# Performance work log

Measured on AMD Instinct MI355X. Metric: run time of the kernel, lower is better.

## Reference

```python
import jax, jax.numpy as jnp
import numpy as np

B, P, ENC = 64, 196, 512
E, H, A, V, L = 1024, 1024, 512, 20000, 25


def setup_inputs() -> dict:
    key = jax.random.key(0)
    ks = jax.random.split(key, 20)
    s = 0.02
    return {
        "encoder_out": jax.random.normal(ks[0], (B, P, ENC), jnp.float32),
        "captions": jax.random.randint(ks[1], (B, L), 0, V),
        "lengths": L,
        # attention MLP
        "W_enc_att": jax.random.normal(ks[2], (ENC, A), jnp.float32) * s,
        "b_enc_att": jnp.zeros((A,), jnp.float32),
        "W_dec_att": jax.random.normal(ks[3], (H, A), jnp.float32) * s,
        "b_dec_att": jnp.zeros((A,), jnp.float32),
        "W_full_att": jax.random.normal(ks[4], (A, 1), jnp.float32) * s,
        "b_full_att": jnp.zeros((1,), jnp.float32),
        # embedding
        "emb_table": jax.random.normal(ks[5], (V, E), jnp.float32) * s,
        # LSTMCell: input = embedding + context -> (E+ENC, 4H)
        "W_ih": jax.random.normal(ks[6], (E + ENC, 4 * H), jnp.float32) * s,
        "b_ih": jnp.zeros((4 * H,), jnp.float32),
        "W_hh": jax.random.normal(ks[7], (H, 4 * H), jnp.float32) * s,
        "b_hh": jnp.zeros((4 * H,), jnp.float32),
        # init states
        "W_init_h": jax.random.normal(ks[8], (ENC, H), jnp.float32) * s,
        "b_init_h": jnp.zeros((H,), jnp.float32),
        "W_init_c": jax.random.normal(ks[9], (ENC, H), jnp.float32) * s,
        "b_init_c": jnp.zeros((H,), jnp.float32),
        # gate + output proj
        "W_fbeta": jax.random.normal(ks[10], (H, ENC), jnp.float32) * s,
        "b_fbeta": jnp.zeros((ENC,), jnp.float32),
        "W_fc": jax.random.normal(ks[11], (H, V), jnp.float32) * s,
        "b_fc": jnp.zeros((V,), jnp.float32),
    }


def _decode(encoder_out, W_enc_att, b_enc_att, W_dec_att, b_dec_att,
            W_full_att, b_full_att, emb_table, W_ih, b_ih, W_hh, b_hh,
            W_init_h, b_init_h, W_init_c, b_init_c, W_fbeta, b_fbeta,
            W_fc, b_fc, captions, T):
    # precompute encoder-side attention projection (constant across timesteps)
    att_enc = encoder_out @ W_enc_att + b_enc_att          # (B, P, A)
    mean_feat = encoder_out.mean(axis=1)                   # (B, ENC)
    h0 = mean_feat @ W_init_h + b_init_h
    c0 = mean_feat @ W_init_c + b_init_c
    embeddings = emb_table[captions[:, :T]]                # (B, T, E)
    xs = jnp.swapaxes(embeddings, 0, 1)                    # (T, B, E)

    def step(carry, emb_t):
        h, c = carry
        att_dec = h @ W_dec_att + b_dec_att                # (B, A)
        energy = (jax.nn.relu(att_enc + att_dec[:, None, :]) @ W_full_att
                  + b_full_att)[..., 0]                    # (B, P)
        alpha = jax.nn.softmax(energy, axis=1)
        context = jnp.einsum('bp,bpe->be', alpha, encoder_out)
        gate = jax.nn.sigmoid(h @ W_fbeta + b_fbeta)       # (B, ENC)
        x = jnp.concatenate([emb_t, gate * context], axis=1)
        gates = x @ W_ih + b_ih + h @ W_hh + b_hh          # (B, 4H)
        i, f, g, o = jnp.split(gates, 4, axis=1)           # torch order i,f,g,o
        c = jax.nn.sigmoid(f) * c + jax.nn.sigmoid(i) * jnp.tanh(g)
        h = jax.nn.sigmoid(o) * jnp.tanh(c)
        preds = h @ W_fc + b_fc                            # dropout = identity (eval)
        return (h, c), (preds, alpha)

    _, (preds, alphas) = jax.lax.scan(step, (h0, c0), xs)
    predictions = jnp.swapaxes(preds, 0, 1)                # (B, T, V)
    alphas = jnp.swapaxes(alphas, 0, 1)                    # (B, T, P)
    return predictions, alphas


def reference(encoder_out, captions, lengths, W_enc_att, b_enc_att, W_dec_att,
              b_dec_att, W_full_att, b_full_att, emb_table, W_ih, b_ih, W_hh,
              b_hh, W_init_h, b_init_h, W_init_c, b_init_c, W_fbeta, b_fbeta,
              W_fc, b_fc):
    T = int(lengths) - 1
    return _decode(encoder_out, W_enc_att, b_enc_att, W_dec_att, b_dec_att,
                   W_full_att, b_full_att, emb_table, W_ih, b_ih, W_hh, b_hh,
                   W_init_h, b_init_h, W_init_c, b_init_c, W_fbeta, b_fbeta,
                   W_fc, b_fc, captions, T)
```

## Files before the change

### kernel.cpp

```cpp
#include <hip/hip_runtime.h>
#include <hip/hip_bf16.h>

#define BB 64
#define PP 196
#define ENCD 512
#define ED 1024
#define HD 1024
#define AD 512
#define VD 20000
#define TT 24
#define VPAD 20096
#define NS 8

typedef __attribute__((ext_vector_type(8))) short short8;
typedef __attribute__((ext_vector_type(4))) short short4v;
typedef __attribute__((ext_vector_type(4))) float f32x4;

__device__ __forceinline__ unsigned short f2bf(float f) {
    unsigned u = __builtin_bit_cast(unsigned, f);
    u = (u + 0x7FFFu + ((u >> 16) & 1u)) >> 16;
    return (unsigned short)u;
}
__device__ __forceinline__ void split2(float v, unsigned short& h, unsigned short& l) {
    h = f2bf(v);
    float hf = __builtin_bit_cast(float, ((unsigned)h) << 16);
    l = f2bf(v - hf);
}

__global__ __launch_bounds__(256) void split_w_kernel(
    const float* __restrict__ W, unsigned short* __restrict__ oh,
    unsigned short* __restrict__ ol, int N, int Npad, int coff, int Nlaunch) {
    int n = blockIdx.x * 256 + threadIdx.x;
    if (n >= Nlaunch) return;
    int kc = blockIdx.y;
    short8 vh, vl;
    #pragma unroll
    for (int j = 0; j < 8; ++j) {
        float v = (n < N) ? W[(size_t)(kc * 8 + j) * N + n] : 0.f;
        unsigned short h, l; split2(v, h, l);
        vh[j] = (short)h; vl[j] = (short)l;
    }
    size_t o = ((size_t)kc * Npad + coff + n) * 8;
    *(short8*)(oh + o) = vh; *(short8*)(ol + o) = vl;
}

__global__ __launch_bounds__(128) void embed_split_kernel(
    const int* __restrict__ captions, const float* __restrict__ table,
    unsigned short* __restrict__ eh, unsigned short* __restrict__ el) {
    int t = blockIdx.x, b = blockIdx.y;
    int kc = threadIdx.x;
    int tok = captions[b * 25 + t];
    const float* row = table + (size_t)tok * ED;
    short8 vh, vl;
    #pragma unroll
    for (int j = 0; j < 8; ++j) {
        unsigned short h, l; split2(row[kc * 8 + j], h, l);
        vh[j] = (short)h; vl[j] = (short)l;
    }
    size_t o = ((size_t)t * 128 * 64 + (size_t)kc * 64 + b) * 8;
    *(short8*)(eh + o) = vh; *(short8*)(el + o) = vl;
}

__global__ __launch_bounds__(512) void mean_kernel(const float* __restrict__ enc,
                                                   float* __restrict__ mf) {
    int b = blockIdx.x; int e = threadIdx.x;
    const float* base = enc + (size_t)b * PP * ENCD + e;
    float s = 0.f;
    #pragma unroll 4
    for (int p = 0; p < PP; ++p) s += base[(size_t)p * ENCD];
    mf[b * ENCD + e] = s * (1.f / PP);
}

__global__ __launch_bounds__(256) void init_hc_kernel(
    const float* __restrict__ mf,
    const float* __restrict__ Wh, const float* __restrict__ bh,
    const float* __restrict__ Wc, const float* __restrict__ bc,
    unsigned short* __restrict__ hc_h, unsigned short* __restrict__ hc_l,
    float* __restrict__ c0) {
    int b = blockIdx.x;
    int isC = blockIdx.y;
    const float* W    = isC ? Wc : Wh;
    const float* bias = isC ? bc : bh;
    __shared__ float smf[ENCD];
    for (int i = threadIdx.x; i < ENCD; i += 256) smf[i] = mf[b * ENCD + i];
    __syncthreads();
    #pragma unroll
    for (int jj = 0; jj < 4; ++jj) {
        int j = threadIdx.x + jj * 256;
        float acc = bias[j];
        for (int k = 0; k < ENCD; ++k) acc += smf[k] * W[(size_t)k * HD + j];
        if (isC) c0[b * HD + j] = acc;
        else {
            unsigned short h, l; split2(acc, h, l);
            size_t o = ((size_t)(j >> 3) * 64 + b) * 8 + (j & 7);
            hc_h[o] = h; hc_l[o] = l;
        }
    }
}

__global__ __launch_bounds__(256) void mfma_gemm_bigf(
    const float* __restrict__ Ap,
    const unsigned short* __restrict__ Bh, const unsigned short* __restrict__ Bl,
    const float* __restrict__ bias, float* __restrict__ C,
    int N, int Npad, int K, int Mtiles, int Ntiles, int inner_m) {
    __shared__ __align__(16) short lds[32768];
    short* Ahs = lds;
    short* Als = lds + 8192;
    short* Bhs = lds + 16384;
    short* Bls = lds + 24576;
    int tid = threadIdx.x, lane = tid & 63, w = tid >> 6;
    int nwg = Mtiles * Ntiles;
    int orig = blockIdx.x;
    int q = nwg >> 3, r = nwg & 7;
    int xcd = orig & 7;
    int basew = (xcd < r) ? xcd * (q + 1) : r * (q + 1) + (xcd - r) * q;
    int wg = basew + (orig >> 3);
    int mt, nt;
    if (inner_m) { mt = wg % Mtiles; nt = wg / Mtiles; }
    else         { nt = wg % Ntiles; mt = wg / Ntiles; }
    int m0 = mt * 128, n0 = nt * 128;
    int wr = w >> 1, wc = w & 1;
    f32x4 acc[4][4];
    #pragma unroll
    for (int i = 0; i < 4; ++i)
        #pragma unroll
        for (int j = 0; j < 4; ++j) acc[i][j] = (f32x4){0.f, 0.f, 0.f, 0.f};
    int nsteps = K >> 6;
    float4 va[8];
    short8 rb[2][4];
    auto load_step = [&](int s) {
        int k0 = s * 64, kc0 = s * 8;
        #pragma unroll
        for (int it = 0; it < 8; ++it) {
            int idx = it * 256 + tid; int m = idx >> 4, k4 = idx & 15;
            va[it] = *(const float4*)(Ap + (size_t)(m0 + m) * K + k0 + k4 * 4);
        }
        #pragma unroll
        for (int it = 0; it < 4; ++it) {
            int g = w * 4 + it; int kcl = g >> 1; int rb0 = (g & 1) * 64;
            size_t gb = ((size_t)(kc0 + kcl) * Npad + n0 + rb0 + lane) * 8;
            rb[0][it] = *(const short8*)(Bh + gb);
            rb[1][it] = *(const short8*)(Bl + gb);
        }
    };
    load_step(0);
    for (int s = 0; s < nsteps; ++s) {
        __syncthreads();
        #pragma unroll
        for (int it = 0; it < 8; ++it) {
            int idx = it * 256 + tid; int m = idx >> 4, k4 = idx & 15;
            int kc = k4 >> 1, jh = (k4 & 1) * 4;
            float vv[4] = {va[it].x, va[it].y, va[it].z, va[it].w};
            short4v hv, lv;
            #pragma unroll
            for (int qq = 0; qq < 4; ++qq) {
                unsigned short h, l; split2(vv[qq], h, l);
                hv[qq] = (short)h; lv[qq] = (short)l;
            }
            int o = kc * 1024 + ((m ^ kc) << 3) + jh;
            *(short4v*)(Ahs + o) = hv;
            *(short4v*)(Als + o) = lv;
        }
        #pragma unroll
        for (int it = 0; it < 4; ++it) {
            int g = w * 4 + it; int kcl = g >> 1; int rb0 = (g & 1) * 64;
            int o = (kcl * 128 + rb0 + lane) * 8;
            *(short8*)(Bhs + o) = rb[0][it];
            *(short8*)(Bls + o) = rb[1][it];
        }
        __syncthreads();
        if (s + 1 < nsteps) load_step(s + 1);
        #pragma unroll
        for (int ks = 0; ks < 2; ++ks) {
            int kq = ks * 4 + (lane >> 4);
            short8 afh[4], afl[4], bfh[4], bfl[4];
            #pragma unroll
            for (int mi = 0; mi < 4; ++mi) {
                int row = wr * 64 + mi * 16 + (lane & 15);
                int o = kq * 1024 + ((row ^ kq) << 3);
                afh[mi] = *(const short8*)(Ahs + o);
                afl[mi] = *(const short8*)(Als + o);
            }
            #pragma unroll
            for (int ni = 0; ni < 4; ++ni) {
                int o = (kq * 128 + wc * 64 + ni * 16 + (lane & 15)) * 8;
                bfh[ni] = *(const short8*)(Bhs + o);
                bfl[ni] = *(const short8*)(Bls + o);
            }
            #pragma unroll
            for (int mi = 0; mi < 4; ++mi)
                #pragma unroll
                for (int ni = 0; ni < 4; ++ni) {
                    acc[mi][ni] = __builtin_amdgcn_mfma_f32_16x16x32_bf16(afh[mi], bfh[ni], acc[mi][ni], 0, 0, 0);
                    acc[mi][ni] = __builtin_amdgcn_mfma_f32_16x16x32_bf16(afh[mi], bfl[ni], acc[mi][ni], 0, 0, 0);
                    acc[mi][ni] = __builtin_amdgcn_mfma_f32_16x16x32_bf16(afl[mi], bfh[ni], acc[mi][ni], 0, 0, 0);
                }
        }
    }
    #pragma unroll
    for (int mi = 0; mi < 4; ++mi) {
        int rrow = m0 + wr * 64 + mi * 16 + ((lane >> 4) << 2);
        #pragma unroll
        for (int ni = 0; ni < 4; ++ni) {
            int c = n0 + wc * 64 + ni * 16 + (lane & 15);
            if (c < N) {
                float bv = bias ? bias[c] : 0.f;
                #pragma unroll
                for (int qq = 0; qq < 4; ++qq)
                    C[(size_t)(rrow + qq) * N + c] = acc[mi][ni][qq] + bv;
            }
        }
    }
}

__global__ __launch_bounds__(256) void mfma_gemm_small(
    const unsigned short* __restrict__ A0h, const unsigned short* __restrict__ A0l,
    const unsigned short* __restrict__ A1h, const unsigned short* __restrict__ A1l,
    const unsigned short* __restrict__ A2h, const unsigned short* __restrict__ A2l,
    int c0, int c1,
    const unsigned short* __restrict__ B0h, const unsigned short* __restrict__ B0l,
    const unsigned short* __restrict__ B1h, const unsigned short* __restrict__ B1l,
    int bc0, float* __restrict__ out, int Npad, int steps) {
    __shared__ __align__(16) short lds[24576];
    short* Ahs = lds;
    short* Als = lds + 4096;
    short* Bhs = lds + 8192;
    short* Bls = lds + 16384;
    int tid = threadIdx.x, lane = tid & 63, w = tid >> 6;
    int n0 = blockIdx.x * 128;
    int kc_base = blockIdx.y * steps * 8;
    out += (size_t)blockIdx.y * 64 * Npad;
    f32x4 acc[4][2];
    #pragma unroll
    for (int i = 0; i < 4; ++i)
        #pragma unroll
        for (int j = 0; j < 2; ++j) acc[i][j] = (f32x4){0.f, 0.f, 0.f, 0.f};
    short8 raa[2][2], rbb[2][4];
    auto load_step = [&](int s) {
        int kc0 = kc_base + s * 8;
        #pragma unroll
        for (int it = 0; it < 2; ++it) {
            int kcl = w * 2 + it; int kcg = kc0 + kcl;
            const unsigned short *ph, *pl; size_t off;
            if (kcg < c0)       { ph = A0h; pl = A0l; off = ((size_t)kcg * 64 + lane) * 8; }
            else if (kcg < c1)  { ph = A1h; pl = A1l; off = ((size_t)(kcg - c0) * 64 + lane) * 8; }
            else                { ph = A2h; pl = A2l; off = ((size_t)(kcg - c1) * 64 + lane) * 8; }
            raa[0][it] = *(const short8*)(ph + off);
            raa[1][it] = *(const short8*)(pl + off);
        }
        #pragma unroll
        for (int it = 0; it < 4; ++it) {
            int g = w * 4 + it; int kcl = g >> 1; int cb = (g & 1) * 64; int kcg = kc0 + kcl;
            const unsigned short *ph, *pl; size_t off;
            if (kcg < bc0) { ph = B0h; pl = B0l; off = ((size_t)kcg * Npad + n0 + cb + lane) * 8; }
            else           { ph = B1h; pl = B1l; off = ((size_t)(kcg - bc0) * Npad + n0 + cb + lane) * 8; }
            rbb[0][it] = *(const short8*)(ph + off);
            rbb[1][it] = *(const short8*)(pl + off);
        }
    };
    load_step(0);
    for (int s = 0; s < steps; ++s) {
        __syncthreads();
        #pragma unroll
        for (int it = 0; it < 2; ++it) {
            int kcl = w * 2 + it; int o = (kcl * 64 + lane) * 8;
            *(short8*)(Ahs + o) = raa[0][it];
            *(short8*)(Als + o) = raa[1][it];
        }
        #pragma unroll
        for (int it = 0; it < 4; ++it) {
            int g = w * 4 + it; int kcl = g >> 1; int cb = (g & 1) * 64;
            int o = (kcl * 128 + cb + lane) * 8;
            *(short8*)(Bhs + o) = rbb[0][it];
            *(short8*)(Bls + o) = rbb[1][it];
        }
        __syncthreads();
        if (s + 1 < steps) load_step(s + 1);
        #pragma unroll
        for (int ks = 0; ks < 2; ++ks) {
            int kq = ks * 4 + (lane >> 4);
            short8 afh[4], afl[4], bfh[2], bfl[2];
            #pragma unroll
            for (int mi = 0; mi < 4; ++mi) {
                int o = (kq * 64 + mi * 16 + (lane & 15)) * 8;
                afh[mi] = *(const short8*)(Ahs + o);
                afl[mi] = *(const short8*)(Als + o);
            }
            #pragma unroll
            for (int ni = 0; ni < 2; ++ni) {
                int o = (kq * 128 + w * 32 + ni * 16 + (lane & 15)) * 8;
                bfh[ni] = *(const short8*)(Bhs + o);
                bfl[ni] = *(const short8*)(Bls + o);
            }
            #pragma unroll
            for (int mi = 0; mi < 4; ++mi)
                #pragma unroll
                for (int ni = 0; ni < 2; ++ni) {
                    acc[mi][ni] = __builtin_amdgcn_mfma_f32_16x16x32_bf16(afh[mi], bfh[ni], acc[mi][ni], 0, 0, 0);
                    acc[mi][ni] = __builtin_amdgcn_mfma_f32_16x16x32_bf16(afh[mi], bfl[ni], acc[mi][ni], 0, 0, 0);
                    acc[mi][ni] = __builtin_amdgcn_mfma_f32_16x16x32_bf16(afl[mi], bfh[ni], acc[mi][ni], 0, 0, 0);
                }
        }
    }
    #pragma unroll
    for (int mi = 0; mi < 4; ++mi) {
        int rrow = mi * 16 + ((lane >> 4) << 2);
        #pragma unroll
        for (int ni = 0; ni < 2; ++ni) {
            int c = n0 + w * 32 + ni * 16 + (lane & 15);
            #pragma unroll
            for (int qq = 0; qq < 4; ++qq)
                out[(size_t)(rrow + qq) * Npad + c] = acc[mi][ni][qq];
        }
    }
}

__global__ __launch_bounds__(1024) void energy_softmax_kernel(
    const float* __restrict__ att_enc, const float* __restrict__ adg,
    const float* __restrict__ b_dec, const float* __restrict__ Wfull,
    float* __restrict__ alpha_out, int t) {
    int b = blockIdx.x; int tid = threadIdx.x;
    __shared__ float sdec[AD], sw[AD], sE[256], red[256];
    if (tid < AD) {
        float s = b_dec[tid];
        #pragma unroll
        for (int ks = 0; ks < NS; ++ks) s += adg[((size_t)ks * BB + b) * 1024 + tid];
        sdec[tid] = s;
        sw[tid] = Wfull[tid];
    }
    __syncthreads();
    int w = tid >> 6, lane = tid & 63;
    float4 sd0 = *(const float4*)&sdec[lane * 8];
    float4 sd1 = *(const float4*)&sdec[lane * 8 + 4];
    float4 sw0 = *(const float4*)&sw[lane * 8];
    float4 sw1 = *(const float4*)&sw[lane * 8 + 4];
    for (int p = w; p < PP; p += 16) {
        const float* row = att_enc + ((size_t)b * PP + p) * AD + lane * 8;
        float4 v0 = *(const float4*)row;
        float4 v1 = *(const float4*)(row + 4);
        float part = fmaxf(v0.x + sd0.x, 0.f) * sw0.x + fmaxf(v0.y + sd0.y, 0.f) * sw0.y +
                     fmaxf(v0.z + sd0.z, 0.f) * sw0.z + fmaxf(v0.w + sd0.w, 0.f) * sw0.w +
                     fmaxf(v1.x + sd1.x, 0.f) * sw1.x + fmaxf(v1.y + sd1.y, 0.f) * sw1.y +
                     fmaxf(v1.z + sd1.z, 0.f) * sw1.z + fmaxf(v1.w + sd1.w, 0.f) * sw1.w;
        #pragma unroll
        for (int off = 32; off > 0; off >>= 1) part += __shfl_down(part, off, 64);
        if (lane == 0) sE[p] = part;
    }
    __syncthreads();
    float myE = (tid < PP) ? sE[tid] : -1e30f;
    if (tid < 256) red[tid] = myE;
    __syncthreads();
    for (int s = 128; s > 0; s >>= 1) {
        if (tid < s) red[tid] = fmaxf(red[tid], red[tid + s]);
        __syncthreads();
    }
    float mx = red[0];
    __syncthreads();
    float ex = (tid < PP) ? __expf(myE - mx) : 0.f;
    if (tid < 256) red[tid] = ex;
    __syncthreads();
    for (int s = 128; s > 0; s >>= 1) {
        if (tid < s) red[tid] += red[tid + s];
        __syncthreads();
    }
    if (tid < PP) alpha_out[((size_t)b * TT + t) * PP + tid] = ex * (1.f / red[0]);
}

__global__ __launch_bounds__(128) void context_gate_kernel(
    const float* __restrict__ enc, const float* __restrict__ alpha,
    const float* __restrict__ adg, const float* __restrict__ b_fbeta,
    unsigned short* __restrict__ x2h, unsigned short* __restrict__ x2l, int t) {
    int b = blockIdx.x;
    int e = blockIdx.y * 128 + threadIdx.x;
    __shared__ float sal[PP];
    for (int i = threadIdx.x; i < PP; i += 128)
        sal[i] = alpha[((size_t)b * TT + t) * PP + i];
    __syncthreads();
    const float* basep = enc + (size_t)b * PP * ENCD + e;
    float s = 0.f;
    #pragma unroll 4
    for (int p = 0; p < PP; ++p) s += sal[p] * basep[(size_t)p * ENCD];
    float gpre = b_fbeta[e];
    #pragma unroll
    for (int ks = 0; ks < NS; ++ks) gpre += adg[((size_t)ks * BB + b) * 1024 + AD + e];
    float gate = 1.f / (1.f + __expf(-gpre));
    unsigned short h, l; split2(gate * s, h, l);
    size_t o = ((size_t)(e >> 3) * 64 + b) * 8 + (e & 7);
    x2h[o] = h; x2l[o] = l;
}

__global__ __launch_bounds__(256) void lstm_kernel(
    const float* __restrict__ gp, const float* __restrict__ b_ih,
    const float* __restrict__ b_hh, float* __restrict__ c,
    unsigned short* __restrict__ hc_h, unsigned short* __restrict__ hc_l,
    float* __restrict__ h_all, int t) {
    int b = blockIdx.x;
    int j = blockIdx.y * 256 + threadIdx.x;
    float gi = b_ih[j] + b_hh[j];
    float gf = b_ih[1024 + j] + b_hh[1024 + j];
    float gg = b_ih[2048 + j] + b_hh[2048 + j];
    float go = b_ih[3072 + j] + b_hh[3072 + j];
    #pragma unroll
    for (int ks = 0; ks < NS; ++ks) {
        const float* g = gp + ((size_t)ks * BB + b) * 4096;
        gi += g[j]; gf += g[1024 + j]; gg += g[2048 + j]; go += g[3072 + j];
    }
    float si = 1.f / (1.f + __expf(-gi));
    float sf = 1.f / (1.f + __expf(-gf));
    float so = 1.f / (1.f + __expf(-go));
    float cn = sf * c[b * HD + j] + si * tanhf(gg);
    c[b * HD + j] = cn;
    float hn = so * tanhf(cn);
    unsigned short h, l; split2(hn, h, l);
    size_t o1 = ((size_t)(j >> 3) * 64 + b) * 8 + (j & 7);
    hc_h[o1] = h; hc_l[o1] = l;
    h_all[((size_t)b * TT + t) * HD + j] = hn;
}

extern "C" void kernel_launch(void* const* d_in, const int* in_sizes, int n_in,
                              void* d_out, int out_size, void* d_ws, size_t ws_size,
                              hipStream_t stream) {
    const float* enc      = (const float*)d_in[0];
    const int*   captions = (const int*)d_in[1];
    const float* W_enc    = (const float*)d_in[3];
    const float* b_enc    = (const float*)d_in[4];
    const float* W_dec    = (const float*)d_in[5];
    const float* b_dec    = (const float*)d_in[6];
    const float* W_full   = (const float*)d_in[7];
    const float* table    = (const float*)d_in[9];
    const float* W_ih     = (const float*)d_in[10];
    const float* b_ih     = (const float*)d_in[11];
    const float* W_hh     = (const float*)d_in[12];
    const float* b_hh     = (const float*)d_in[13];
    const float* W_init_h = (const float*)d_in[14];
    const float* b_init_h = (const float*)d_in[15];
    const float* W_init_c = (const float*)d_in[16];
    const float* b_init_c = (const float*)d_in[17];
    const float* W_fbeta  = (const float*)d_in[18];
    const float* b_fbeta  = (const float*)d_in[19];
    const float* W_fc     = (const float*)d_in[20];
    const float* b_fc     = (const float*)d_in[21];

    float* preds  = (float*)d_out;
    float* alphas = (float*)d_out + (size_t)BB * TT * VD;

    char* base = (char*)d_ws;
    size_t off = 0;
    auto take = [&](size_t b) { void* r = (void*)(base + off); off += (b + 255) & ~(size_t)255; return r; };
    float* att_enc = (float*)take((size_t)12544 * 512 * 4);
    unsigned short* wih_h  = (unsigned short*)take((size_t)192 * 4096 * 8 * 2);
    unsigned short* wih_l  = (unsigned short*)take((size_t)192 * 4096 * 8 * 2);
    unsigned short* whh_h  = (unsigned short*)take((size_t)128 * 4096 * 8 * 2);
    unsigned short* whh_l  = (unsigned short*)take((size_t)128 * 4096 * 8 * 2);
    unsigned short* watt_h = (unsigned short*)take((size_t)128 * 1024 * 8 * 2);
    unsigned short* watt_l = (unsigned short*)take((size_t)128 * 1024 * 8 * 2);
    unsigned short* wenc_h = (unsigned short*)take((size_t)64 * 512 * 8 * 2);
    unsigned short* wenc_l = (unsigned short*)take((size_t)64 * 512 * 8 * 2);
    unsigned short* emb_h  = (unsigned short*)take((size_t)TT * 128 * 64 * 8 * 2);
    unsigned short* emb_l  = (unsigned short*)take((size_t)TT * 128 * 64 * 8 * 2);
    float* adg = (float*)take((size_t)NS * BB * 1024 * 4);
    float* gp  = (float*)take((size_t)NS * BB * 4096 * 4);
    unsigned short* wfc_h = (unsigned short*)(base);
    unsigned short* wfc_l = (unsigned short*)(base + (size_t)128 * VPAD * 8 * 2);
    float* c_buf = (float*)take((size_t)BB * HD * 4);
    float* mf    = (float*)take((size_t)BB * ENCD * 4);
    unsigned short* x2c_h = (unsigned short*)take((size_t)64 * 64 * 8 * 2);
    unsigned short* x2c_l = (unsigned short*)take((size_t)64 * 64 * 8 * 2);
    unsigned short* hc_h  = (unsigned short*)take((size_t)128 * 64 * 8 * 2);
    unsigned short* hc_l  = (unsigned short*)take((size_t)128 * 64 * 8 * 2);
    float* h_all = (float*)take((size_t)TT * BB * HD * 4);

    const int BIG = 1 << 20;

    split_w_kernel<<<dim3(2, 64), 256, 0, stream>>>(W_enc, wenc_h, wenc_l, 512, 512, 0, 512);
    split_w_kernel<<<dim3(2, 128), 256, 0, stream>>>(W_dec, watt_h, watt_l, 512, 1024, 0, 512);
    split_w_kernel<<<dim3(2, 128), 256, 0, stream>>>(W_fbeta, watt_h, watt_l, 512, 1024, 512, 512);
    split_w_kernel<<<dim3(16, 192), 256, 0, stream>>>(W_ih, wih_h, wih_l, 4096, 4096, 0, 4096);
    split_w_kernel<<<dim3(16, 128), 256, 0, stream>>>(W_hh, whh_h, whh_l, 4096, 4096, 0, 4096);
    embed_split_kernel<<<dim3(TT, BB), 128, 0, stream>>>(captions, table, emb_h, emb_l);
    mean_kernel<<<BB, 512, 0, stream>>>(enc, mf);
    init_hc_kernel<<<dim3(BB, 2), 256, 0, stream>>>(mf, W_init_h, b_init_h, W_init_c, b_init_c,
                                                    hc_h, hc_l, c_buf);
    mfma_gemm_bigf<<<392, 256, 0, stream>>>(enc, wenc_h, wenc_l, b_enc, att_enc,
                                            512, 512, 512, 98, 4, 0);

    for (int t = 0; t < TT; ++t) {
        mfma_gemm_small<<<dim3(8, NS), 256, 0, stream>>>(
            hc_h, hc_l, nullptr, nullptr, nullptr, nullptr, BIG, BIG,
            watt_h, watt_l, nullptr, nullptr, BIG, adg, 1024, 2);
        energy_softmax_kernel<<<BB, 1024, 0, stream>>>(att_enc, adg, b_dec, W_full, alphas, t);
        context_gate_kernel<<<dim3(BB, 4), 128, 0, stream>>>(enc, alphas, adg, b_fbeta,
                                                             x2c_h, x2c_l, t);
        mfma_gemm_small<<<dim3(32, NS), 256, 0, stream>>>(
            emb_h + (size_t)t * 128 * 64 * 8, emb_l + (size_t)t * 128 * 64 * 8,
            x2c_h, x2c_l, hc_h, hc_l, 128, 192,
            wih_h, wih_l, whh_h, whh_l, 192, gp, 4096, 5);
        lstm_kernel<<<dim3(BB, 4), 256, 0, stream>>>(gp, b_ih, b_hh, c_buf, hc_h, hc_l, h_all, t);
    }

    split_w_kernel<<<dim3(79, 128), 256, 0, stream>>>(W_fc, wfc_h, wfc_l, VD, VPAD, 0, VPAD);
    mfma_gemm_bigf<<<1884, 256, 0, stream>>>(h_all, wfc_h, wfc_l, b_fc, preds,
                                             VD, VPAD, 1024, 12, 157, 1);
}
```

Measured before the change: 1.514 ms.

## Hoist embedding input projection out of loop and fuse gate GEMM with LSTM

Result: slower. 1.565 ms (+3.4%).

```diff
diff --git a/kernel.cpp b/kernel.cpp
--- a/kernel.cpp
+++ b/kernel.cpp
@@ -10,11 +10,13 @@
 #define VD 20000
 #define TT 24
 #define VPAD 20096
-#define NS 8
+#define NSA 4
 
 typedef __attribute__((ext_vector_type(8))) short short8;
 typedef __attribute__((ext_vector_type(4))) short short4v;
 typedef __attribute__((ext_vector_type(4))) float f32x4;
+
+__device__ __forceinline__ float sigf(float x) { return 1.f / (1.f + __expf(-x)); }
 
 __device__ __forceinline__ unsigned short f2bf(float f) {
     unsigned u = __builtin_bit_cast(unsigned, f);
@@ -29,14 +31,16 @@
 
 __global__ __launch_bounds__(256) void split_w_kernel(
     const float* __restrict__ W, unsigned short* __restrict__ oh,
-    unsigned short* __restrict__ ol, int N, int Npad, int coff, int Nlaunch) {
+    unsigned short* __restrict__ ol, int N , int Npad, int coff,
+    int Nlaunch, int rowoff, int perm) {
     int n = blockIdx.x * 256 + threadIdx.x;
     if (n >= Nlaunch) return;
     int kc = blockIdx.y;
+    int src = perm ? ((n & 3) * 1024 + (n >> 2)) : n;
     short8 vh, vl;
     #pragma unroll
     for (int j = 0; j < 8; ++j) {
-        float v = (n < N) ? W[(size_t)(kc * 8 + j) * N + n] : 0.f;
+        float v = (src < N) ? W[(size_t)(rowoff + kc * 8 + j) * N + src] : 0.f;
         unsigned short h, l; split2(v, h, l);
         vh[j] = (short)h; vl[j] = (short)l;
     }
@@ -44,21 +48,22 @@
     *(short8*)(oh + o) = vh; *(short8*)(ol + o) = vl;
 }
 
-__global__ __launch_bounds__(128) void embed_split_kernel(
+__global__ __launch_bounds__(256) void embed_f32_kernel(
     const int* __restrict__ captions, const float* __restrict__ table,
-    unsigned short* __restrict__ eh, unsigned short* __restrict__ el) {
+    float* __restrict__ emb_f) {
     int t = blockIdx.x, b = blockIdx.y;
-    int kc = threadIdx.x;
     int tok = captions[b * 25 + t];
-    const float* row = table + (size_t)tok * ED;
-    short8 vh, vl;
-    #pragma unroll
-    for (int j = 0; j < 8; ++j) {
-        unsigned short h, l; split2(row[kc * 8 + j], h, l);
-        vh[j] = (short)h; vl[j] = (short)l;
-    }
-    size_t o = ((size_t)t * 128 * 64 + (size_t)kc * 64 + b) * 8;
-    *(short8*)(eh + o) = vh; *(short8*)(el + o) = vl;
+    const float4* src = (const float4*)(table + (size_t)tok * ED);
+    float4* dst = (float4*)(emb_f + ((size_t)t * BB + b) * ED);
+    dst[threadIdx.x] = src[threadIdx.x];
+}
+
+__global__ __launch_bounds__(256) void bias_perm_kernel(
+    const float* __restrict__ b_ih, const float* __restrict__ b_hh,
+    float* __restrict__ out) {
+    int n = blockIdx.x * 256 + threadIdx.x;
+    int src = (n & 3) * 1024 + (n >> 2);
+    out[n] = b_ih[src] + b_hh[src];
 }
 
 __global__ __launch_bounds__(512) void mean_kernel(const float* __restrict__ enc,
@@ -215,12 +220,8 @@
 
 __global__ __launch_bounds__(256) void mfma_gemm_small(
     const unsigned short* __restrict__ A0h, const unsigned short* __restrict__ A0l,
-    const unsigned short* __restrict__ A1h, const unsigned short* __restrict__ A1l,
-    const unsigned short* __restrict__ A2h, const unsigned short* __restrict__ A2l,
-    int c0, int c1,
     const unsigned short* __restrict__ B0h, const unsigned short* __restrict__ B0l,
-    const unsigned short* __restrict__ B1h, const unsigned short* __restrict__ B1l,
-    int bc0, float* __restrict__ out, int Npad, int steps) {
+    float* __restrict__ out, int Npad, int steps) {
     __shared__ __align__(16) short lds[24576];
     short* Ahs = lds;
     short* Als = lds + 4096;
@@ -240,22 +241,16 @@
         int kc0 = kc_base + s * 8;
         #pragma unroll
         for (int it = 0; it < 2; ++it) {
-            int kcl = w * 2 + it; int kcg = kc0 + kcl;
-            const unsigned short *ph, *pl; size_t off;
-            if (kcg < c0)       { ph = A0h; pl = A0l; off = ((size_t)kcg * 64 + lane) * 8; }
-            else if (kcg < c1)  { ph = A1h; pl = A1l; off = ((size_t)(kcg - c0) * 64 + lane) * 8; }
-            else                { ph = A2h; pl = A2l; off = ((size_t)(kcg - c1) * 64 + lane) * 8; }
-            raa[0][it] = *(const short8*)(ph + off);
-            raa[1][it] = *(const short8*)(pl + off);
+            int kcl = w * 2 + it; size_t off = ((size_t)(kc0 + kcl) * 64 + lane) * 8;
+            raa[0][it] = *(const short8*)(A0h + off);
+            raa[1][it] = *(const short8*)(A0l + off);
         }
         #pragma unroll
         for (int it = 0; it < 4; ++it) {
-            int g = w * 4 + it; int kcl = g >> 1; int cb = (g & 1) * 64; int kcg = kc0 + kcl;
-            const unsigned short *ph, *pl; size_t off;
-            if (kcg < bc0) { ph = B0h; pl = B0l; off = ((size_t)kcg * Npad + n0 + cb + lane) * 8; }
-            else           { ph = B1h; pl = B1l; off = ((size_t)(kcg - bc0) * Npad + n0 + cb + lane) * 8; }
-            rbb[0][it] = *(const short8*)(ph + off);
-            rbb[1][it] = *(const short8*)(pl + off);
+            int g = w * 4 + it; int kcl = g >> 1; int cb = (g & 1) * 64;
+            size_t off = ((size_t)(kc0 + kcl) * Npad + n0 + cb + lane) * 8;
+            rbb[0][it] = *(const short8*)(B0h + off);
+            rbb[1][it] = *(const short8*)(B0l + off);
         }
     };
     load_step(0);
@@ -324,7 +319,7 @@
     if (tid < AD) {
         float s = b_dec[tid];
         #pragma unroll
-        for (int ks = 0; ks < NS; ++ks) s += adg[((size_t)ks * BB + b) * 1024 + tid];
+        for (int ks = 0; ks < NSA; ++ks) s += adg[((size_t)ks * BB + b) * 5120 + tid];
         sdec[tid] = s;
         sw[tid] = Wfull[tid];
     }
@@ -382,39 +377,117 @@
     for (int p = 0; p < PP; ++p) s += sal[p] * basep[(size_t)p * ENCD];
     float gpre = b_fbeta[e];
     #pragma unroll
-    for (int ks = 0; ks < NS; ++ks) gpre += adg[((size_t)ks * BB + b) * 1024 + AD + e];
-    float gate = 1.f / (1.f + __expf(-gpre));
+    for (int ks = 0; ks < NSA; ++ks) gpre += adg[((size_t)ks * BB + b) * 5120 + 512 + e];
+    float gate = sigf(gpre);
     unsigned short h, l; split2(gate * s, h, l);
     size_t o = ((size_t)(e >> 3) * 64 + b) * 8 + (e & 7);
     x2h[o] = h; x2l[o] = l;
 }
 
-__global__ __launch_bounds__(256) void lstm_kernel(
-    const float* __restrict__ gp, const float* __restrict__ b_ih,
-    const float* __restrict__ b_hh, float* __restrict__ c,
-    unsigned short* __restrict__ hc_h, unsigned short* __restrict__ hc_l,
-    float* __restrict__ h_all, int t) {
-    int b = blockIdx.x;
-    int j = blockIdx.y * 256 + threadIdx.x;
-    float gi = b_ih[j] + b_hh[j];
-    float gf = b_ih[1024 + j] + b_hh[1024 + j];
-    float gg = b_ih[2048 + j] + b_hh[2048 + j];
-    float go = b_ih[3072 + j] + b_hh[3072 + j];
-    #pragma unroll
-    for (int ks = 0; ks < NS; ++ks) {
-        const float* g = gp + ((size_t)ks * BB + b) * 4096;
-        gi += g[j]; gf += g[1024 + j]; gg += g[2048 + j]; go += g[3072 + j];
-    }
-    float si = 1.f / (1.f + __expf(-gi));
-    float sf = 1.f / (1.f + __expf(-gf));
-    float so = 1.f / (1.f + __expf(-go));
-    float cn = sf * c[b * HD + j] + si * tanhf(gg);
-    c[b * HD + j] = cn;
-    float hn = so * tanhf(cn);
-    unsigned short h, l; split2(hn, h, l);
-    size_t o1 = ((size_t)(j >> 3) * 64 + b) * 8 + (j & 7);
-    hc_h[o1] = h; hc_l[o1] = l;
-    h_all[((size_t)b * TT + t) * HD + j] = hn;
+__global__ __launch_bounds__(128) void gates_lstm_kernel(
+    const unsigned short* __restrict__ Ah, const unsigned short* __restrict__ Al,
+    const unsigned short* __restrict__ Bh, const unsigned short* __restrict__ Bl,
+    const float* __restrict__ pregates, const float* __restrict__ adg,
+    float* __restrict__ c, unsigned short* __restrict__ hc_h,
+    unsigned short* __restrict__ hc_l, float* __restrict__ h_all, int t) {
+    __shared__ __align__(16) short lds[12288];
+    __shared__ float gl[64][36];
+    short* Ahs = lds;
+    short* Als = lds + 4096;
+    short* Bhs = lds + 8192;
+    short* Bls = lds + 10240;
+    int tid = threadIdx.x, lane = tid & 63, w = tid >> 6;
+    int n0 = blockIdx.x * 32;
+    f32x4 acc[4];
+    #pragma unroll
+    for (int i = 0; i < 4; ++i) acc[i] = (f32x4){0.f, 0.f, 0.f, 0.f};
+    short8 ra[2][4], rb[2][2];
+    auto load_step = [&](int s) {
+        int kc0 = s * 8;
+        #pragma unroll
+        for (int it = 0; it < 4; ++it) {
+            int idx = it * 128 + tid; int kcl = idx >> 6, row = idx & 63;
+            size_t off = ((size_t)(kc0 + kcl) * 64 + row) * 8;
+            ra[0][it] = *(const short8*)(Ah + off);
+            ra[1][it] = *(const short8*)(Al + off);
+        }
+        #pragma unroll
+        for (int it = 0; it < 2; ++it) {
+            int idx = it * 128 + tid; int kcl = idx >> 5, col = idx & 31;
+            size_t off = ((size_t)(kc0 + kcl) * 4096 + n0 + col) * 8;
+            rb[0][it] = *(const short8*)(Bh + off);
+            rb[1][it] = *(const short8*)(Bl + off);
+        }
+    };
+    load_step(0);
+    for (int s = 0; s < 8; ++s) {
+        __syncthreads();
+        #pragma unroll
+        for (int it = 0; it < 4; ++it) {
+            int idx = it * 128 + tid; int kcl = idx >> 6, row = idx & 63;
+            int o = (kcl * 64 + row) * 8;
+            *(short8*)(Ahs + o) = ra[0][it];
+            *(short8*)(Als + o) = ra[1][it];
+        }
+        #pragma unroll
+        for (int it = 0; it < 2; ++it) {
+            int idx = it * 128 + tid; int kcl = idx >> 5, col = idx & 31;
+            int o = (kcl * 32 + col) * 8;
+            *(short8*)(Bhs + o) = rb[0][it];
+            *(short8*)(Bls + o) = rb[1][it];
+        }
+        __syncthreads();
+        if (s + 1 < 8) load_step(s + 1);
+        #pragma unroll
+        for (int ks = 0; ks < 2; ++ks) {
+            int kq = ks * 4 + (lane >> 4);
+            short8 afh[4], afl[4], bfh, bfl;
+            #pragma unroll
+            for (int mi = 0; mi < 4; ++mi) {
+                int o = (kq * 64 + mi * 16 + (lane & 15)) * 8;
+                afh[mi] = *(const short8*)(Ahs + o);
+                afl[mi] = *(const short8*)(Als + o);
+            }
+            int ob = (kq * 32 + w * 16 + (lane & 15)) * 8;
+            bfh = *(const short8*)(Bhs + ob);
+            bfl = *(const short8*)(Bls + ob);
+            #pragma unroll
+            for (int mi = 0; mi < 4; ++mi) {
+                acc[mi] = __builtin_amdgcn_mfma_f32_16x16x32_bf16(afh[mi], bfh, acc[mi], 0, 0, 0);
+                acc[mi] = __builtin_amdgcn_mfma_f32_16x16x32_bf16(afh[mi], bfl, acc[mi], 0, 0, 0);
+                acc[mi] = __builtin_amdgcn_mfma_f32_16x16x32_bf16(afl[mi], bfh, acc[mi], 0, 0, 0);
+            }
+        }
+    }
+    int cL = w * 16 + (lane & 15);
+    #pragma unroll
+    for (int mi = 0; mi < 4; ++mi) {
+        #pragma unroll
+        for (int qq = 0; qq < 4; ++qq) {
+            int b = mi * 16 + ((lane >> 4) << 2) + qq;
+            float val = acc[mi][qq] + pregates[((size_t)(t * 64 + b)) * 4096 + n0 + cL];
+            #pragma unroll
+            for (int ks = 0; ks < NSA; ++ks)
+                val += adg[((size_t)ks * BB + b) * 5120 + 1024 + n0 + cL];
+            gl[b][cL] = val;
+        }
+    }
+    __syncthreads();
+    #pragma unroll
+    for (int i = 0; i < 4; ++i) {
+        int idx = tid + i * 128;
+        int b = idx >> 3, jl = idx & 7;
+        float iG = gl[b][4 * jl + 0], fG = gl[b][4 * jl + 1];
+        float gG = gl[b][4 * jl + 2], oG = gl[b][4 * jl + 3];
+        int j = (n0 >> 2) + jl;
+        float cn = sigf(fG) * c[b * HD + j] + sigf(iG) * tanhf(gG);
+        c[b * HD + j] = cn;
+        float hn = sigf(oG) * tanhf(cn);
+        unsigned short h, l; split2(hn, h, l);
+        size_t o1 = ((size_t)(j >> 3) * 64 + b) * 8 + (j & 7);
+        hc_h[o1] = h; hc_l[o1] = l;
+        h_all[((size_t)b * TT + t) * HD + j] = hn;
+    }
 }
 
 extern "C" void kernel_launch(void* const* d_in, const int* in_sizes, int n_in,
@@ -448,20 +521,20 @@
     size_t off = 0;
     auto take = [&](size_t b) { void* r = (void*)(base + off); off += (b + 255) & ~(size_t)255; return r; };
     float* att_enc = (float*)take((size_t)12544 * 512 * 4);
-    unsigned short* wih_h  = (unsigned short*)take((size_t)192 * 4096 * 8 * 2);
-    unsigned short* wih_l  = (unsigned short*)take((size_t)192 * 4096 * 8 * 2);
-    unsigned short* whh_h  = (unsigned short*)take((size_t)128 * 4096 * 8 * 2);
-    unsigned short* whh_l  = (unsigned short*)take((size_t)128 * 4096 * 8 * 2);
-    unsigned short* watt_h = (unsigned short*)take((size_t)128 * 1024 * 8 * 2);
-    unsigned short* watt_l = (unsigned short*)take((size_t)128 * 1024 * 8 * 2);
+    unsigned short* wbig_h = (unsigned short*)take((size_t)128 * 5120 * 8 * 2);
+    unsigned short* wbig_l = (unsigned short*)take((size_t)128 * 5120 * 8 * 2);
+    unsigned short* wih2_h = (unsigned short*)take((size_t)64 * 4096 * 8 * 2);
+    unsigned short* wih2_l = (unsigned short*)take((size_t)64 * 4096 * 8 * 2);
+    float* pregates = (float*)take((size_t)TT * BB * 4096 * 4);
+    float* adg      = (float*)take((size_t)NSA * BB * 5120 * 4);
+    unsigned short* wfc_h = (unsigned short*)(base);
+    unsigned short* wfc_l = (unsigned short*)(base + (size_t)128 * VPAD * 8 * 2);
+    unsigned short* wih1_h = (unsigned short*)take((size_t)128 * 4096 * 8 * 2);
+    unsigned short* wih1_l = (unsigned short*)take((size_t)128 * 4096 * 8 * 2);
     unsigned short* wenc_h = (unsigned short*)take((size_t)64 * 512 * 8 * 2);
     unsigned short* wenc_l = (unsigned short*)take((size_t)64 * 512 * 8 * 2);
-    unsigned short* emb_h  = (unsigned short*)take((size_t)TT * 128 * 64 * 8 * 2);
-    unsigned short* emb_l  = (unsigned short*)take((size_t)TT * 128 * 64 * 8 * 2);
-    float* adg = (float*)take((size_t)NS * BB * 1024 * 4);
-    float* gp  = (float*)take((size_t)NS * BB * 4096 * 4);
-    unsigned short* wfc_h = (unsigned short*)(base);
-    unsigned short* wfc_l = (unsigned short*)(base + (size_t)128 * VPAD * 8 * 2);
+    float* emb_f    = (float*)take((size_t)TT * BB * ED * 4);
+    float* biasp    = (float*)take((size_t)4096 * 4);
     float* c_buf = (float*)take((size_t)BB * HD * 4);
     float* mf    = (float*)take((size_t)BB * ENCD * 4);
     unsigned short* x2c_h = (unsigned short*)take((size_t)64 * 64 * 8 * 2);
@@ -470,35 +543,33 @@
     unsigned short* hc_l  = (unsigned short*)take((size_t)128 * 64 * 8 * 2);
     float* h_all = (float*)take((size_t)TT * BB * HD * 4);
 
-    const int BIG = 1 << 20;
-
-    split_w_kernel<<<dim3(2, 64), 256, 0, stream>>>(W_enc, wenc_h, wenc_l, 512, 512, 0, 512);
-    split_w_kernel<<<dim3(2, 128), 256, 0, stream>>>(W_dec, watt_h, watt_l, 512, 1024, 0, 512);
-    split_w_kernel<<<dim3(2, 128), 256, 0, stream>>>(W_fbeta, watt_h, watt_l, 512, 1024, 512, 512);
-    split_w_kernel<<<dim3(16, 192), 256, 0, stream>>>(W_ih, wih_h, wih_l, 4096, 4096, 0, 4096);
-    split_w_kernel<<<dim3(16, 128), 256, 0, stream>>>(W_hh, whh_h, whh_l, 4096, 4096, 0, 4096);
-    embed_split_kernel<<<dim3(TT, BB), 128, 0, stream>>>(captions, table, emb_h, emb_l);
+    split_w_kernel<<<dim3(2, 64), 256, 0, stream>>>(W_enc, wenc_h, wenc_l, 512, 512, 0, 512, 0, 0);
+    split_w_kernel<<<dim3(2, 128), 256, 0, stream>>>(W_dec, wbig_h, wbig_l, 512, 5120, 0, 512, 0, 0);
+    split_w_kernel<<<dim3(2, 128), 256, 0, stream>>>(W_fbeta, wbig_h, wbig_l, 512, 5120, 512, 512, 0, 0);
+    split_w_kernel<<<dim3(16, 128), 256, 0, stream>>>(W_hh, wbig_h, wbig_l, 4096, 5120, 1024, 4096, 0, 1);
+    split_w_kernel<<<dim3(16, 128), 256, 0, stream>>>(W_ih, wih1_h, wih1_l, 4096, 4096, 0, 4096, 0, 1);
+    split_w_kernel<<<dim3(16, 64), 256, 0, stream>>>(W_ih, wih2_h, wih2_l, 4096, 4096, 0, 4096, 1024, 1);
+    bias_perm_kernel<<<16, 256, 0, stream>>>(b_ih, b_hh, biasp);
+    embed_f32_kernel<<<dim3(TT, BB), 256, 0, stream>>>(captions, table, emb_f);
     mean_kernel<<<BB, 512, 0, stream>>>(enc, mf);
     init_hc_kernel<<<dim3(BB, 2), 256, 0, stream>>>(mf, W_init_h, b_init_h, W_init_c, b_init_c,
                                                     hc_h, hc_l, c_buf);
     mfma_gemm_bigf<<<392, 256, 0, stream>>>(enc, wenc_h, wenc_l, b_enc, att_enc,
                                             512, 512, 512, 98, 4, 0);
+    mfma_gemm_bigf<<<384, 256, 0, stream>>>(emb_f, wih1_h, wih1_l, biasp, pregates,
+                                            4096, 4096, 1024, 12, 32, 1);
 
     for (int t = 0; t < TT; ++t) {
-        mfma_gemm_small<<<dim3(8, NS), 256, 0, stream>>>(
-            hc_h, hc_l, nullptr, nullptr, nullptr, nullptr, BIG, BIG,
-            watt_h, watt_l, nullptr, nullptr, BIG, adg, 1024, 2);
+        mfma_gemm_small<<<dim3(40, NSA), 256, 0, stream>>>(hc_h, hc_l, wbig_h, wbig_l,
+                                                           adg, 5120, 4);
         energy_softmax_kernel<<<BB, 1024, 0, stream>>>(att_enc, adg, b_dec, W_full, alphas, t);
         context_gate_kernel<<<dim3(BB, 4), 128, 0, stream>>>(enc, alphas, adg, b_fbeta,
                                                              x2c_h, x2c_l, t);
-        mfma_gemm_small<<<dim3(32, NS), 256, 0, stream>>>(
-            emb_h + (size_t)t * 128 * 64 * 8, emb_l + (size_t)t * 128 * 64 * 8,
-            x2c_h, x2c_l, hc_h, hc_l, 128, 192,
-            wih_h, wih_l, whh_h, whh_l, 192, gp, 4096, 5);
-        lstm_kernel<<<dim3(BB, 4), 256, 0, stream>>>(gp, b_ih, b_hh, c_buf, hc_h, hc_l, h_all, t);
-    }
-
-    split_w_kernel<<<dim3(79, 128), 256, 0, stream>>>(W_fc, wfc_h, wfc_l, VD, VPAD, 0, VPAD);
+        gates_lstm_kernel<<<128, 128, 0, stream>>>(x2c_h, x2c_l, wih2_h, wih2_l,
+                                                   pregates, adg, c_buf, hc_h, hc_l, h_all, t);
+    }
+
+    split_w_kernel<<<dim3(79, 128), 256, 0, stream>>>(W_fc, wfc_h, wfc_l, VD, VPAD, 0, VPAD, 0, 0);
     mfma_gemm_bigf<<<1884, 256, 0, stream>>>(h_all, wfc_h, wfc_l, b_fc, preds,
                                              VD, VPAD, 1024, 12, 157, 1);
 }
```
